# Kernel optimization log

Measured on AMD Instinct MI355X. Metric: run time of the kernel, lower is better.

The kernel has to match this reference:

```python
import jax, jax.numpy as jnp
import numpy as np

B = 131072
D = 64          # d_model
T = 4           # num_tiles
TEMP = 0.5


def setup_inputs() -> dict:
    key = jax.random.key(0)
    ks = jax.random.split(key, 16)
    s = 0.02
    return {
        "a_vec": jax.random.normal(ks[0], (B, D), dtype=jnp.float32),
        "b_vec": jax.random.normal(ks[1], (B, D), dtype=jnp.float32),
        "pos_encoding": jax.random.normal(ks[2], (B, 8), dtype=jnp.float32),
        # router: Linear(2D+8 -> D), GELU, Linear(D -> T)
        "Wr1": jax.random.normal(ks[3], (2 * D + 8, D), dtype=jnp.float32) * s,
        "br1": jnp.zeros((D,), dtype=jnp.float32),
        "Wr2": jax.random.normal(ks[4], (D, T), dtype=jnp.float32) * s,
        "br2": jnp.zeros((T,), dtype=jnp.float32),
        # tile nets: per-tile Linear(2D -> 2D), GELU, Linear(2D -> D)
        "W1": jax.random.normal(ks[5], (T, 2 * D, 2 * D), dtype=jnp.float32) * s,
        "b1": jnp.zeros((T, 2 * D), dtype=jnp.float32),
        "W2": jax.random.normal(ks[6], (T, 2 * D, D), dtype=jnp.float32) * s,
        "b2": jnp.zeros((T, D), dtype=jnp.float32),
    }


def _router(x, Wr1, br1, Wr2, br2):
    h = jax.nn.gelu(x @ Wr1 + br1, approximate=False)  # torch nn.GELU is exact
    return (h @ Wr2 + br2) / TEMP


def reference(a_vec, b_vec, pos_encoding, Wr1, br1, Wr2, br2, W1, b1, W2, b2):
    pair = jnp.concatenate([a_vec, b_vec], axis=-1)            # (B, 2D)

    # Routing 1 uses pair; routing 2 uses flipped pair. Both expert passes
    # consume `pair` (faithful to the original code, which feeds pair both times).
    idx1 = jnp.argmax(_router(jnp.concatenate([pair, pos_encoding], -1),
                              Wr1, br1, Wr2, br2), axis=-1)    # (B,)
    pair_flip = jnp.concatenate([b_vec, a_vec], axis=-1)
    idx2 = jnp.argmax(_router(jnp.concatenate([pair_flip, pos_encoding], -1),
                              Wr1, br1, Wr2, br2), axis=-1)    # (B,)

    # Run all tiles on every sample (small T), then gather the routed output.
    h = jax.nn.gelu(jnp.einsum('bi,tij->btj', pair, W1) + b1, approximate=False)  # (B,T,2D)
    out_all = jnp.einsum('bth,thd->btd', h, W2) + b2                              # (B,T,D)

    out1 = jnp.take_along_axis(out_all, idx1[:, None, None], axis=1)[:, 0]
    out2 = jnp.take_along_axis(out_all, idx2[:, None, None], axis=1)[:, 0]
    return out1, out2
```

## Files before the change

### kernel.cpp

```cpp
#include <hip/hip_runtime.h>

#define B_N 131072

using bfrag_t = __attribute__((ext_vector_type(8))) short;
using acc_t   = __attribute__((ext_vector_type(4))) float;
using v4f     = __attribute__((ext_vector_type(4))) float;
using i32x4_t = __attribute__((ext_vector_type(4))) int;

__device__ __forceinline__ unsigned short f2bf(float f) {
  unsigned int u = __float_as_uint(f);
  u += 0x7FFFu + ((u >> 16) & 1u);
  return (unsigned short)(u >> 16);
}

__device__ __forceinline__ unsigned int pk2bf(float x, float y) {
  return (unsigned int)f2bf(x) | ((unsigned int)f2bf(y) << 16);
}

__device__ __forceinline__ void gload_lds16(const void* g, void* l) {
  __builtin_amdgcn_global_load_lds((const __attribute__((address_space(1))) void*)g,
                                   (__attribute__((address_space(3))) void*)l, 16, 0, 0);
}

__device__ __forceinline__ float gelu_f(float x) {
  float ax = fabsf(x) * 0.70710678118654752f;
  float t  = __builtin_amdgcn_rcpf(fmaf(0.3275911f, ax, 1.0f));
  float p  = fmaf(1.061405429f, t, -1.453152027f);
  p = fmaf(p, t, 1.421413741f);
  p = fmaf(p, t, -0.284496736f);
  p = fmaf(p, t, 0.254829592f);
  p = p * t;
  float e  = __expf(-ax * ax);
  float er = fmaf(-p, e, 1.0f);
  er = (x < 0.0f) ? -er : er;
  return 0.5f * x * (1.0f + er);
}

#define QP_F(v, CTRL) __int_as_float(__builtin_amdgcn_mov_dpp(__float_as_int(v), (CTRL), 0xF, 0xF, false))
#define QP_I(v, CTRL) __builtin_amdgcn_mov_dpp((v), (CTRL), 0xF, 0xF, false)

__global__ __launch_bounds__(256) void prepack2_k(
    const float* __restrict__ Wr1, const float* __restrict__ br1,
    const float* __restrict__ Wr2, const float* __restrict__ br2,
    const float* __restrict__ W1, const float* __restrict__ W2,
    float* __restrict__ RW, short* __restrict__ W1s, short* __restrict__ W2s,
    unsigned int* __restrict__ counts) {
  int gt = blockIdx.x * 256 + threadIdx.x;
  if (gt < 4) counts[gt] = 0u;
  for (int idx = gt; idx < 142 * 64; idx += 16384) {
    int row = idx >> 6, j = idx & 63; float val;
    if (row < 136)      val = Wr1[row * 64 + j];
    else if (row == 136) val = br1[j];
    else if (row < 141) val = Wr2[(row - 137) * 64 + j];
    else                val = (j < 4) ? br2[j] : 0.0f;
    RW[idx] = val;
  }
  for (int ch = gt; ch < 8192; ch += 16384) {
    int t = ch >> 11, r = (ch >> 4) & 127, c = ch & 15;
    const float* src = W1 + t * 16384 + r;
    short* dst = W1s + (t * 128 + r) * 128 + ((c ^ (r & 15)) * 8);
    #pragma unroll
    for (int m = 0; m < 8; m++) dst[m] = (short)f2bf(src[(c * 8 + m) * 128]);
  }
  for (int ch = gt; ch < 4096; ch += 16384) {
    int t = ch >> 10, d = (ch >> 4) & 63, c = ch & 15;
    const float* src = W2 + t * 8192 + d;
    short* dst = W2s + (t * 64 + d) * 128 + ((c ^ (d & 15)) * 8);
    #pragma unroll
    for (int m = 0; m < 8; m++) dst[m] = (short)f2bf(src[(c * 8 + m) * 64]);
  }
}

__global__ __launch_bounds__(256) void router11_k(
    const float* __restrict__ a, const float* __restrict__ b,
    const float* __restrict__ pos, const float* __restrict__ RW,
    unsigned char* __restrict__ r1, unsigned char* __restrict__ r2,
    unsigned int* __restrict__ gcounts) {
  __shared__ float SB[17984];
  __shared__ unsigned int hcnt[4];
  const int XO = 9088, PO = 17408;
  int tid = threadIdx.x, wave = tid >> 6, lane = tid & 63;
  int s0 = blockIdx.x * 64;
  if (tid < 4) hcnt[tid] = 0u;

  for (int it = 0; it < 9; it++) {
    int cb = it * 256 + wave * 64;
    if (cb < 2272) {
      int chunk = cb + lane;
      if (chunk < 2272) gload_lds16(RW + chunk * 4, (char*)SB + cb * 16);
    }
  }
  #pragma unroll
  for (int it = 0; it < 8; it++) {
    int idx = it * 256 + tid;
    int s = idx >> 5, c = idx & 31;
    const float* src = (c < 16) ? (a + (size_t)(s0 + s) * 64 + c * 4)
                                : (b + (size_t)(s0 + s) * 64 + (c - 16) * 4);
    v4f v = *(const v4f*)src;
    float* dst = SB + XO + s * 130 + ((c < 16) ? c * 4 : 64 + (c - 16) * 4);
    *(float2*)dst = float2{v[0], v[1]};
    *(float2*)(dst + 2) = float2{v[2], v[3]};
  }
  #pragma unroll
  for (int r = 0; r < 2; r++) {
    int idx = r * 256 + tid;
    int s = idx >> 3, c = idx & 7;
    SB[PO + s * 9 + c] = pos[(size_t)(s0 + s) * 8 + c];
  }
  __syncthreads();

  int sp = tid >> 3, jg = tid & 7;
  const float* Xs0 = SB + XO + sp * 130;
  const float* Xs1 = SB + XO + (sp + 32) * 130;
  v4f acc1[2][2], acc2[2][2];
  {
    v4f bi0 = *(const v4f*)(SB + 136 * 64 + jg * 8);
    v4f bi1 = *(const v4f*)(SB + 136 * 64 + jg * 8 + 4);
    acc1[0][0] = bi0; acc1[0][1] = bi1; acc1[1][0] = bi0; acc1[1][1] = bi1;
    acc2[0][0] = bi0; acc2[0][1] = bi1; acc2[1][0] = bi0; acc2[1][1] = bi1;
  }
  #pragma unroll 4
  for (int i = 0; i < 64; i++) {
    float xa0 = Xs0[i], xb0 = Xs0[64 + i];
    float xa1 = Xs1[i], xb1 = Xs1[64 + i];
    const v4f* w = (const v4f*)(SB + i * 64 + jg * 8);
    v4f w0 = w[0], w1 = w[1];
    v4f A0 = {xa0, xa0, xa0, xa0}, B0 = {xb0, xb0, xb0, xb0};
    v4f A1 = {xa1, xa1, xa1, xa1}, B1 = {xb1, xb1, xb1, xb1};
    acc1[0][0] = __builtin_elementwise_fma(A0, w0, acc1[0][0]);
    acc1[0][1] = __builtin_elementwise_fma(A0, w1, acc1[0][1]);
    acc2[0][0] = __builtin_elementwise_fma(B0, w0, acc2[0][0]);
    acc2[0][1] = __builtin_elementwise_fma(B0, w1, acc2[0][1]);
    acc1[1][0] = __builtin_elementwise_fma(A1, w0, acc1[1][0]);
    acc1[1][1] = __builtin_elementwise_fma(A1, w1, acc1[1][1]);
    acc2[1][0] = __builtin_elementwise_fma(B1, w0, acc2[1][0]);
    acc2[1][1] = __builtin_elementwise_fma(B1, w1, acc2[1][1]);
  }
  #pragma unroll 4
  for (int i = 0; i < 64; i++) {
    float xa0 = Xs0[i], xb0 = Xs0[64 + i];
    float xa1 = Xs1[i], xb1 = Xs1[64 + i];
    const v4f* w = (const v4f*)(SB + (64 + i) * 64 + jg * 8);
    v4f w0 = w[0], w1 = w[1];
    v4f A0 = {xa0, xa0, xa0, xa0}, B0 = {xb0, xb0, xb0, xb0};
    v4f A1 = {xa1, xa1, xa1, xa1}, B1 = {xb1, xb1, xb1, xb1};
    acc1[0][0] = __builtin_elementwise_fma(B0, w0, acc1[0][0]);
    acc1[0][1] = __builtin_elementwise_fma(B0, w1, acc1[0][1]);
    acc2[0][0] = __builtin_elementwise_fma(A0, w0, acc2[0][0]);
    acc2[0][1] = __builtin_elementwise_fma(A0, w1, acc2[0][1]);
    acc1[1][0] = __builtin_elementwise_fma(B1, w0, acc1[1][0]);
    acc1[1][1] = __builtin_elementwise_fma(B1, w1, acc1[1][1]);
    acc2[1][0] = __builtin_elementwise_fma(A1, w0, acc2[1][0]);
    acc2[1][1] = __builtin_elementwise_fma(A1, w1, acc2[1][1]);
  }
  #pragma unroll 2
  for (int i = 0; i < 8; i++) {
    float p0 = SB[PO + sp * 9 + i];
    float p1 = SB[PO + (sp + 32) * 9 + i];
    const v4f* w = (const v4f*)(SB + (128 + i) * 64 + jg * 8);
    v4f w0 = w[0], w1 = w[1];
    v4f P0 = {p0, p0, p0, p0}, P1 = {p1, p1, p1, p1};
    acc1[0][0] = __builtin_elementwise_fma(P0, w0, acc1[0][0]);
    acc1[0][1] = __builtin_elementwise_fma(P0, w1, acc1[0][1]);
    acc2[0][0] = __builtin_elementwise_fma(P0, w0, acc2[0][0]);
    acc2[0][1] = __builtin_elementwise_fma(P0, w1, acc2[0][1]);
    acc1[1][0] = __builtin_elementwise_fma(P1, w0, acc1[1][0]);
    acc1[1][1] = __builtin_elementwise_fma(P1, w1, acc1[1][1]);
    acc2[1][0] = __builtin_elementwise_fma(P1, w0, acc2[1][0]);
    acc2[1][1] = __builtin_elementwise_fma(P1, w1, acc2[1][1]);
  }
  #pragma unroll
  for (int s = 0; s < 2; s++)
    #pragma unroll
    for (int e = 0; e < 2; e++)
      #pragma unroll
      for (int c = 0; c < 4; c++) {
        acc1[s][e][c] = gelu_f(acc1[s][e][c]);
        acc2[s][e][c] = gelu_f(acc2[s][e][c]);
      }
  __syncthreads();
  float2* HX2 = (float2*)(SB + XO);
  #pragma unroll
  for (int s = 0; s < 2; s++) {
    int sg = sp + s * 32;
    #pragma unroll
    for (int e = 0; e < 2; e++)
      #pragma unroll
      for (int c = 0; c < 4; c++)
        HX2[sg * 66 + jg * 8 + e * 4 + c] = float2{acc1[s][e][c], acc2[s][e][c]};
  }
  __syncthreads();
  int sL = tid >> 2, m = tid & 3;
  float l1 = SB[141 * 64 + m], l2 = l1;
  #pragma unroll 8
  for (int j = 0; j < 64; j++) {
    float2 h = HX2[sL * 66 + j];
    float wv = SB[137 * 64 + j * 4 + m];
    l1 = fmaf(h.x, wv, l1);
    l2 = fmaf(h.y, wv, l2);
  }
  float o1 = QP_F(l1, 0xB1), o2 = QP_F(l2, 0xB1);
  bool odd = (m & 1) != 0;
  float vhi1 = odd ? l1 : o1, vlo1 = odd ? o1 : l1;
  float vhi2 = odd ? l2 : o2, vlo2 = odd ? o2 : l2;
  int ihi = m | 1, ilo = m & ~1;
  bool w1c = vhi1 > vlo1, w2c = vhi2 > vlo2;
  float bv1 = w1c ? vhi1 : vlo1;  int bi1 = w1c ? ihi : ilo;
  float bv2 = w2c ? vhi2 : vlo2;  int bi2 = w2c ? ihi : ilo;
  float p1s = QP_F(bv1, 0x4E); int q1s = QP_I(bi1, 0x4E);
  float p2s = QP_F(bv2, 0x4E); int q2s = QP_I(bi2, 0x4E);
  bool hi2 = (m & 2) != 0;
  float uhi1 = hi2 ? bv1 : p1s, ulo1 = hi2 ? p1s : bv1;
  int   jhi1 = hi2 ? bi1 : q1s, jlo1 = hi2 ? q1s : bi1;
  float uhi2 = hi2 ? bv2 : p2s, ulo2 = hi2 ? p2s : bv2;
  int   jhi2 = hi2 ? bi2 : q2s, jlo2 = hi2 ? q2s : bi2;
  int idx1 = (uhi1 > ulo1) ? jhi1 : jlo1;
  int idx2 = (uhi2 > ulo2) ? jhi2 : jlo2;
  if (m == 0) {
    r1[s0 + sL] = (unsigned char)idx1;
    r2[s0 + sL] = (unsigned char)idx2;
    atomicAdd(&hcnt[idx1], 1u);
    atomicAdd(&hcnt[idx2], 1u);
  }
  __syncthreads();
  if (tid < 4) atomicAdd(gcounts + tid, hcnt[tid]);
}

__global__ __launch_bounds__(256) void offsets_k(
    const unsigned int* __restrict__ counts, unsigned int* __restrict__ table,
    unsigned int* __restrict__ cursors, unsigned int* __restrict__ list) {
  __shared__ unsigned int ps[5], cnt[4];
  int tid = threadIdx.x;
  if (tid == 0) {
    unsigned int acc = 0;
    for (int t = 0; t < 4; t++) {
      ps[t] = acc;
      unsigned int c = counts[t];
      cnt[t] = c;
      acc += ((c + 127u) >> 7) << 7;
    }
    ps[4] = acc;
    #pragma unroll
    for (int t = 0; t < 5; t++) table[t] = ps[t];
    #pragma unroll
    for (int t = 0; t < 4; t++) cursors[t] = ps[t];
  }
  __syncthreads();
  #pragma unroll
  for (int r = 0; r < 2; r++) {
    int idx = r * 256 + tid;
    int t = idx >> 7, i = idx & 127;
    unsigned int pos = ps[t] + cnt[t] + (unsigned int)i;
    if (pos < ps[t + 1]) list[pos] = 0xFFFFFFFFu;
  }
}

__global__ __launch_bounds__(256) void place_k(
    const unsigned char* __restrict__ r1, const unsigned char* __restrict__ r2,
    unsigned int* __restrict__ cursors, unsigned int* __restrict__ list) {
  __shared__ unsigned int lc[4], lb[4];
  int tid = threadIdx.x;
  if (tid < 4) lc[tid] = 0u;
  __syncthreads();
  int s = blockIdx.x * 256 + tid;
  int e1 = (int)r1[s], e2 = (int)r2[s];
  unsigned int k1 = atomicAdd(&lc[e1], 1u);
  unsigned int k2 = atomicAdd(&lc[e2], 1u);
  __syncthreads();
  if (tid < 4) lb[tid] = atomicAdd(&cursors[tid], lc[tid]);
  __syncthreads();
  list[lb[e1] + k1] = ((unsigned int)s << 1);
  list[lb[e2] + k2] = ((unsigned int)s << 1) | 1u;
}

__global__ __launch_bounds__(256) void expert3_k(
    const float* __restrict__ a, const float* __restrict__ b,
    const short* __restrict__ W1s, const short* __restrict__ W2s,
    const float* __restrict__ b1, const float* __restrict__ b2,
    const unsigned int* __restrict__ table, const unsigned int* __restrict__ list,
    float* __restrict__ out) {
  __shared__ short LB[24576];
  __shared__ unsigned int eLS[128];
  int tid = threadIdx.x;
  int wave = tid >> 6, lane = tid & 63;
  int q = lane >> 4, sm = lane & 15;

  unsigned int p0 = blockIdx.x * 128u;
  unsigned int t1 = table[1], t2 = table[2], t3 = table[3], t4 = table[4];
  if (p0 >= t4) return;
  int t = (p0 >= t1) + (p0 >= t2) + (p0 >= t3);

  if (tid < 128) eLS[tid] = list[p0 + tid];
  __syncthreads();

  #pragma unroll
  for (int r = 0; r < 8; r++) {
    int slot = r * 256 + tid;
    int g = slot >> 10, sg = slot & 1023;
    int f = sg >> 6, l = sg & 63;
    int sgrp = f >> 2, kb = f & 3;
    int ls2 = g * 64 + sgrp * 16 + (l & 15);
    unsigned int e = eLS[ls2];
    int s = (e == 0xFFFFFFFFu) ? 0 : (int)(e >> 1);
    int k = kb * 32 + (l >> 4) * 8;
    const float* src = (k < 64) ? (a + (size_t)s * 64 + k) : (b + (size_t)s * 64 + (k - 64));
    acc_t v0 = *(const acc_t*)(src);
    acc_t v1 = *(const acc_t*)(src + 4);
    i32x4_t pk;
    pk[0] = (int)pk2bf(v0[0], v0[1]);
    pk[1] = (int)pk2bf(v0[2], v0[3]);
    pk[2] = (int)pk2bf(v1[0], v1[1]);
    pk[3] = (int)pk2bf(v1[2], v1[3]);
    *(i32x4_t*)(&LB[slot * 8]) = pk;
  }
  __syncthreads();
  bfrag_t bfrag[2][4];
  #pragma unroll
  for (int g = 0; g < 2; g++)
    #pragma unroll
    for (int kb = 0; kb < 4; kb++)
      bfrag[g][kb] = *(const bfrag_t*)(&LB[((g * 16 + wave * 4 + kb) * 64 + lane) * 8]);

  unsigned int eA = eLS[wave * 16 + sm];
  unsigned int eB = eLS[64 + wave * 16 + sm];
  __syncthreads();

  acc_t zero = {0.f, 0.f, 0.f, 0.f};
  int vb[4];
  #pragma unroll
  for (int kb = 0; kb < 4; kb++) vb[kb] = sm * 256 + (((kb * 4 + q) ^ sm) * 16);
  int addr0 = (((q & 1) * 2) * 16 + sm) * 4;
  int addr1 = addr0 + 64;
  bool hi = (q >> 1) != 0;

  #pragma unroll
  for (int it = 0; it < 12; it++) {
    int cb = it * 256 + wave * 64;
    int chunk = cb + lane;
    const short* gsrc = (chunk < 2048) ? (W1s + t * 16384 + chunk * 8)
                                       : (W2s + t * 8192 + (chunk - 2048) * 8);
    gload_lds16(gsrc, (char*)LB + cb * 16);
  }
  __syncthreads();

  #pragma unroll
  for (int g = 0; g < 2; g++) {
    unsigned int hp[8][2];
    #pragma unroll
    for (int mt = 0; mt < 8; mt++) {
      acc_t c = zero;
      #pragma unroll
      for (int kb = 0; kb < 4; kb++) {
        bfrag_t A = *(const bfrag_t*)((const char*)LB + mt * 4096 + vb[kb]);
        c = __builtin_amdgcn_mfma_f32_16x16x32_bf16(A, bfrag[g][kb], c, 0, 0, 0);
      }
      acc_t bv = *(const acc_t*)(b1 + t * 128 + mt * 16 + q * 4);
      float g0 = gelu_f(c[0] + bv[0]);
      float g1 = gelu_f(c[1] + bv[1]);
      float g2 = gelu_f(c[2] + bv[2]);
      float g3 = gelu_f(c[3] + bv[3]);
      hp[mt][0] = pk2bf(g0, g1);
      hp[mt][1] = pk2bf(g2, g3);
    }
    bfrag_t b2f[4];
    #pragma unroll
    for (int kb2 = 0; kb2 < 4; kb2++) {
      int p00 = __builtin_amdgcn_ds_bpermute(addr0, (int)hp[2 * kb2][0]);
      int p01 = __builtin_amdgcn_ds_bpermute(addr0, (int)hp[2 * kb2][1]);
      int p10 = __builtin_amdgcn_ds_bpermute(addr1, (int)hp[2 * kb2][0]);
      int p11 = __builtin_amdgcn_ds_bpermute(addr1, (int)hp[2 * kb2][1]);
      int q00 = __builtin_amdgcn_ds_bpermute(addr0, (int)hp[2 * kb2 + 1][0]);
      int q01 = __builtin_amdgcn_ds_bpermute(addr0, (int)hp[2 * kb2 + 1][1]);
      int q10 = __builtin_amdgcn_ds_bpermute(addr1, (int)hp[2 * kb2 + 1][0]);
      int q11 = __builtin_amdgcn_ds_bpermute(addr1, (int)hp[2 * kb2 + 1][1]);
      i32x4_t w;
      w[0] = hi ? q00 : p00;
      w[1] = hi ? q01 : p01;
      w[2] = hi ? q10 : p10;
      w[3] = hi ? q11 : p11;
      b2f[kb2] = __builtin_bit_cast(bfrag_t, w);
    }
    unsigned int e = g ? eB : eA;
    bool live = (e != 0xFFFFFFFFu);
    size_t so = ((size_t)(e & 1u)) * B_N + (size_t)(e >> 1);
    float* p = out + so * 64 + q * 4;
    #pragma unroll
    for (int mt2 = 0; mt2 < 4; mt2++) {
      acc_t c = zero;
      #pragma unroll
      for (int kb2 = 0; kb2 < 4; kb2++) {
        bfrag_t A = *(const bfrag_t*)((const char*)LB + 32768 + mt2 * 4096 + vb[kb2]);
        c = __builtin_amdgcn_mfma_f32_16x16x32_bf16(A, b2f[kb2], c, 0, 0, 0);
      }
      acc_t bv = *(const acc_t*)(b2 + t * 64 + mt2 * 16 + q * 4);
      c[0] += bv[0]; c[1] += bv[1]; c[2] += bv[2]; c[3] += bv[3];
      if (live) *(acc_t*)(p + mt2 * 16) = c;
    }
  }
}

extern "C" void kernel_launch(void* const* d_in, const int* in_sizes, int n_in,
                              void* d_out, int out_size, void* d_ws, size_t ws_size,
                              hipStream_t stream) {
  const float* a   = (const float*)d_in[0];
  const float* bv  = (const float*)d_in[1];
  const float* pos = (const float*)d_in[2];
  const float* Wr1 = (const float*)d_in[3];
  const float* br1 = (const float*)d_in[4];
  const float* Wr2 = (const float*)d_in[5];
  const float* br2 = (const float*)d_in[6];
  const float* W1  = (const float*)d_in[7];
  const float* b1  = (const float*)d_in[8];
  const float* W2  = (const float*)d_in[9];
  const float* b2  = (const float*)d_in[10];
  float* out = (float*)d_out;

  unsigned char* r1 = (unsigned char*)d_ws;
  unsigned char* r2 = r1 + B_N;
  float* RW  = (float*)((char*)d_ws + 262144);
  short* W1s = (short*)((char*)d_ws + 298496);
  short* W2s = (short*)((char*)d_ws + 429568);
  unsigned int* counts  = (unsigned int*)((char*)d_ws + 495104);
  unsigned int* cursors = (unsigned int*)((char*)d_ws + 495120);
  unsigned int* table   = (unsigned int*)((char*)d_ws + 495136);
  unsigned int* list    = (unsigned int*)((char*)d_ws + 495168);

  prepack2_k<<<64, 256, 0, stream>>>(Wr1, br1, Wr2, br2, W1, W2, RW, W1s, W2s, counts);
  router11_k<<<B_N / 64, 256, 0, stream>>>(a, bv, pos, RW, r1, r2, counts);
  offsets_k<<<1, 256, 0, stream>>>(counts, table, cursors, list);
  place_k<<<B_N / 256, 256, 0, stream>>>(r1, r2, cursors, list);
  expert3_k<<<2052, 256, 0, stream>>>(a, bv, W1s, W2s, b1, b2, table, list, out);
}
```

Baseline: 249.3 us.

## Pack pair inputs to bf16 in router and fuse offsets into place kernel

The router kernel now also writes a bf16-packed copy of the concatenated a/b pair into workspace. The expert kernel can then gather half as many bytes per routed sample directly into LDS with global_load_lds, instead of reading fp32 inputs. The offsets kernel is removed: place2 computes the prefix table itself, cursors are zeroed in prepack, and the expert kernel derives tile boundaries from counts. This drops one launch and reduces gather traffic, at the cost of extra writes in the router and a dependency on a large enough workspace, with the old path kept as a fallback.

New measurement: 248.0 us. No clear change (-0.6%).

```diff
diff --git a/kernel.cpp b/kernel.cpp
--- a/kernel.cpp
+++ b/kernel.cpp
@@ -44,9 +44,10 @@
     const float* __restrict__ Wr2, const float* __restrict__ br2,
     const float* __restrict__ W1, const float* __restrict__ W2,
     float* __restrict__ RW, short* __restrict__ W1s, short* __restrict__ W2s,
-    unsigned int* __restrict__ counts) {
+    unsigned int* __restrict__ counts, unsigned int* __restrict__ cursors) {
   int gt = blockIdx.x * 256 + threadIdx.x;
   if (gt < 4) counts[gt] = 0u;
+  else if (gt < 8) cursors[gt - 4] = 0u;
   for (int idx = gt; idx < 142 * 64; idx += 16384) {
     int row = idx >> 6, j = idx & 63; float val;
     if (row < 136)      val = Wr1[row * 64 + j];
@@ -71,11 +72,12 @@
   }
 }
 
-__global__ __launch_bounds__(256) void router11_k(
+__global__ __launch_bounds__(256) void router11b_k(
     const float* __restrict__ a, const float* __restrict__ b,
     const float* __restrict__ pos, const float* __restrict__ RW,
     unsigned char* __restrict__ r1, unsigned char* __restrict__ r2,
-    unsigned int* __restrict__ gcounts) {
+    unsigned int* __restrict__ gcounts, unsigned short* __restrict__ pairs16,
+    int dopack) {
   __shared__ float SB[17984];
   __shared__ unsigned int hcnt[4];
   const int XO = 9088, PO = 17408;
@@ -97,9 +99,16 @@
     const float* src = (c < 16) ? (a + (size_t)(s0 + s) * 64 + c * 4)
                                 : (b + (size_t)(s0 + s) * 64 + (c - 16) * 4);
     v4f v = *(const v4f*)src;
-    float* dst = SB + XO + s * 130 + ((c < 16) ? c * 4 : 64 + (c - 16) * 4);
+    int k = (c < 16) ? c * 4 : 64 + (c - 16) * 4;
+    float* dst = SB + XO + s * 130 + k;
     *(float2*)dst = float2{v[0], v[1]};
     *(float2*)(dst + 2) = float2{v[2], v[3]};
+    if (dopack) {
+      uint2 pk;
+      pk.x = pk2bf(v[0], v[1]);
+      pk.y = pk2bf(v[2], v[3]);
+      *(uint2*)((char*)pairs16 + ((size_t)(s0 + s) * 128 + k) * 2) = pk;
+    }
   }
   #pragma unroll
   for (int r = 0; r < 2; r++) {
@@ -226,6 +235,164 @@
   if (tid < 4) atomicAdd(gcounts + tid, hcnt[tid]);
 }
 
+__global__ __launch_bounds__(256) void place2_k(
+    const unsigned char* __restrict__ r1, const unsigned char* __restrict__ r2,
+    const unsigned int* __restrict__ counts, unsigned int* __restrict__ cursors,
+    unsigned int* __restrict__ list) {
+  __shared__ unsigned int lc[4], lb[4], psS[5];
+  int tid = threadIdx.x;
+  if (tid == 0) {
+    unsigned int acc = 0;
+    #pragma unroll
+    for (int t = 0; t < 4; t++) {
+      psS[t] = acc;
+      acc += ((counts[t] + 127u) >> 7) << 7;
+    }
+    psS[4] = acc;
+  }
+  if (tid < 4) lc[tid] = 0u;
+  __syncthreads();
+  int s = blockIdx.x * 256 + tid;
+  int e1 = (int)r1[s], e2 = (int)r2[s];
+  unsigned int k1 = atomicAdd(&lc[e1], 1u);
+  unsigned int k2 = atomicAdd(&lc[e2], 1u);
+  __syncthreads();
+  if (tid < 4) lb[tid] = atomicAdd(&cursors[tid], lc[tid]);
+  __syncthreads();
+  list[psS[e1] + lb[e1] + k1] = ((unsigned int)s << 1);
+  list[psS[e2] + lb[e2] + k2] = ((unsigned int)s << 1) | 1u;
+  if (blockIdx.x < 4) {
+    int t = blockIdx.x;
+    unsigned int cnt = counts[t];
+    unsigned int pad = psS[t + 1] - psS[t] - cnt;
+    if ((unsigned int)tid < pad) list[psS[t] + cnt + tid] = 0xFFFFFFFFu;
+  }
+}
+
+__global__ __launch_bounds__(256) void expert4_k(
+    const unsigned short* __restrict__ pairs16,
+    const short* __restrict__ W1s, const short* __restrict__ W2s,
+    const float* __restrict__ b1, const float* __restrict__ b2,
+    const unsigned int* __restrict__ counts, const unsigned int* __restrict__ list,
+    float* __restrict__ out) {
+  __shared__ short LB[24576];
+  __shared__ unsigned int eLS[128];
+  int tid = threadIdx.x;
+  int wave = tid >> 6, lane = tid & 63;
+  int q = lane >> 4, sm = lane & 15;
+
+  unsigned int c0 = counts[0], c1 = counts[1], c2 = counts[2], c3 = counts[3];
+  unsigned int ps1 = (((c0 + 127u) >> 7) << 7);
+  unsigned int ps2 = ps1 + (((c1 + 127u) >> 7) << 7);
+  unsigned int ps3 = ps2 + (((c2 + 127u) >> 7) << 7);
+  unsigned int ps4 = ps3 + (((c3 + 127u) >> 7) << 7);
+
+  unsigned int p0 = blockIdx.x * 128u;
+  if (p0 >= ps4) return;
+  int t = (p0 >= ps1) + (p0 >= ps2) + (p0 >= ps3);
+
+  if (tid < 128) eLS[tid] = list[p0 + tid];
+  __syncthreads();
+
+  #pragma unroll
+  for (int r = 0; r < 8; r++) {
+    int cb = r * 256 + wave * 64;
+    int slot = cb + lane;
+    int g = slot >> 10, sg = slot & 1023;
+    int f = sg >> 6, l = sg & 63;
+    int sgrp = f >> 2, kb = f & 3;
+    unsigned int e = eLS[g * 64 + sgrp * 16 + (l & 15)];
+    int s = (e == 0xFFFFFFFFu) ? 0 : (int)(e >> 1);
+    int k = kb * 32 + (l >> 4) * 8;
+    gload_lds16((const char*)pairs16 + ((size_t)s * 128 + k) * 2,
+                (char*)LB + cb * 16);
+  }
+  __syncthreads();
+  bfrag_t bfrag[2][4];
+  #pragma unroll
+  for (int g = 0; g < 2; g++)
+    #pragma unroll
+    for (int kb = 0; kb < 4; kb++)
+      bfrag[g][kb] = *(const bfrag_t*)(&LB[((g * 16 + wave * 4 + kb) * 64 + lane) * 8]);
+
+  unsigned int eA = eLS[wave * 16 + sm];
+  unsigned int eB = eLS[64 + wave * 16 + sm];
+  __syncthreads();
+
+  acc_t zero = {0.f, 0.f, 0.f, 0.f};
+  int vb[4];
+  #pragma unroll
+  for (int kb = 0; kb < 4; kb++) vb[kb] = sm * 256 + (((kb * 4 + q) ^ sm) * 16);
+  int addr0 = (((q & 1) * 2) * 16 + sm) * 4;
+  int addr1 = addr0 + 64;
+  bool hi = (q >> 1) != 0;
+
+  #pragma unroll
+  for (int it = 0; it < 12; it++) {
+    int cb = it * 256 + wave * 64;
+    int chunk = cb + lane;
+    const short* gsrc = (chunk < 2048) ? (W1s + t * 16384 + chunk * 8)
+                                       : (W2s + t * 8192 + (chunk - 2048) * 8);
+    gload_lds16(gsrc, (char*)LB + cb * 16);
+  }
+  __syncthreads();
+
+  #pragma unroll
+  for (int g = 0; g < 2; g++) {
+    unsigned int hp[8][2];
+    #pragma unroll
+    for (int mt = 0; mt < 8; mt++) {
+      acc_t c = zero;
+      #pragma unroll
+      for (int kb = 0; kb < 4; kb++) {
+        bfrag_t A = *(const bfrag_t*)((const char*)LB + mt * 4096 + vb[kb]);
+        c = __builtin_amdgcn_mfma_f32_16x16x32_bf16(A, bfrag[g][kb], c, 0, 0, 0);
+      }
+      acc_t bv = *(const acc_t*)(b1 + t * 128 + mt * 16 + q * 4);
+      float g0 = gelu_f(c[0] + bv[0]);
+      float g1 = gelu_f(c[1] + bv[1]);
+      float g2 = gelu_f(c[2] + bv[2]);
+      float g3 = gelu_f(c[3] + bv[3]);
+      hp[mt][0] = pk2bf(g0, g1);
+      hp[mt][1] = pk2bf(g2, g3);
+    }
+    bfrag_t b2f[4];
+    #pragma unroll
+    for (int kb2 = 0; kb2 < 4; kb2++) {
+      int p00 = __builtin_amdgcn_ds_bpermute(addr0, (int)hp[2 * kb2][0]);
+      int p01 = __builtin_amdgcn_ds_bpermute(addr0, (int)hp[2 * kb2][1]);
+      int p10 = __builtin_amdgcn_ds_bpermute(addr1, (int)hp[2 * kb2][0]);
+      int p11 = __builtin_amdgcn_ds_bpermute(addr1, (int)hp[2 * kb2][1]);
+      int q00 = __builtin_amdgcn_ds_bpermute(addr0, (int)hp[2 * kb2 + 1][0]);
+      int q01 = __builtin_amdgcn_ds_bpermute(addr0, (int)hp[2 * kb2 + 1][1]);
+      int q10 = __builtin_amdgcn_ds_bpermute(addr1, (int)hp[2 * kb2 + 1][0]);
+      int q11 = __builtin_amdgcn_ds_bpermute(addr1, (int)hp[2 * kb2 + 1][1]);
+      i32x4_t w;
+      w[0] = hi ? q00 : p00;
+      w[1] = hi ? q01 : p01;
+      w[2] = hi ? q10 : p10;
+      w[3] = hi ? q11 : p11;
+      b2f[kb2] = __builtin_bit_cast(bfrag_t, w);
+    }
+    unsigned int e = g ? eB : eA;
+    bool live = (e != 0xFFFFFFFFu);
+    size_t so = ((size_t)(e & 1u)) * B_N + (size_t)(e >> 1);
+    float* p = out + so * 64 + q * 4;
+    #pragma unroll
+    for (int mt2 = 0; mt2 < 4; mt2++) {
+      acc_t c = zero;
+      #pragma unroll
+      for (int kb2 = 0; kb2 < 4; kb2++) {
+        bfrag_t A = *(const bfrag_t*)((const char*)LB + 32768 + mt2 * 4096 + vb[kb2]);
+        c = __builtin_amdgcn_mfma_f32_16x16x32_bf16(A, b2f[kb2], c, 0, 0, 0);
+      }
+      acc_t bv = *(const acc_t*)(b2 + t * 64 + mt2 * 16 + q * 4);
+      c[0] += bv[0]; c[1] += bv[1]; c[2] += bv[2]; c[3] += bv[3];
+      if (live) *(acc_t*)(p + mt2 * 16) = c;
+    }
+  }
+}
+
 __global__ __launch_bounds__(256) void offsets_k(
     const unsigned int* __restrict__ counts, unsigned int* __restrict__ table,
     unsigned int* __restrict__ cursors, unsigned int* __restrict__ list) {
@@ -424,10 +591,20 @@
   unsigned int* cursors = (unsigned int*)((char*)d_ws + 495120);
   unsigned int* table   = (unsigned int*)((char*)d_ws + 495136);
   unsigned int* list    = (unsigned int*)((char*)d_ws + 495168);
-
-  prepack2_k<<<64, 256, 0, stream>>>(Wr1, br1, Wr2, br2, W1, W2, RW, W1s, W2s, counts);
-  router11_k<<<B_N / 64, 256, 0, stream>>>(a, bv, pos, RW, r1, r2, counts);
-  offsets_k<<<1, 256, 0, stream>>>(counts, table, cursors, list);
-  place_k<<<B_N / 256, 256, 0, stream>>>(r1, r2, cursors, list);
-  expert3_k<<<2052, 256, 0, stream>>>(a, bv, W1s, W2s, b1, b2, table, list, out);
-}
+  unsigned short* pairs16 = (unsigned short*)((char*)d_ws + 2097152);
+
+  bool fast = (ws_size >= (size_t)2097152 + (size_t)B_N * 256);
+
+  prepack2_k<<<64, 256, 0, stream>>>(Wr1, br1, Wr2, br2, W1, W2, RW, W1s, W2s,
+                                     counts, cursors);
+  router11b_k<<<B_N / 64, 256, 0, stream>>>(a, bv, pos, RW, r1, r2, counts,
+                                            pairs16, fast ? 1 : 0);
+  if (fast) {
+    place2_k<<<B_N / 256, 256, 0, stream>>>(r1, r2, counts, cursors, list);
+    expert4_k<<<2052, 256, 0, stream>>>(pairs16, W1s, W2s, b1, b2, counts, list, out);
+  } else {
+    offsets_k<<<1, 256, 0, stream>>>(counts, table, cursors, list);
+    place_k<<<B_N / 256, 256, 0, stream>>>(r1, r2, cursors, list);
+    expert3_k<<<2052, 256, 0, stream>>>(a, bv, W1s, W2s, b1, b2, table, list, out);
+  }
+}
```
